# Kernel optimization log

Hardware: AMD Instinct MI355X
Metric: run time of the kernel (lower is better)

The kernel has to match this reference:

```python
import jax, jax.numpy as jnp
import numpy as np

DIM = 1024
HEADS = 16
HEAD_DIM = DIM // HEADS          # 64
ROT_DIM = max(16, HEAD_DIM // 2) # 32 (already even)
B, S = 1, 2048


def _linear_params(key, scale=0.02):
    w = jax.random.normal(key, (DIM, DIM), dtype=jnp.float32) * scale
    b = jnp.zeros((DIM,), dtype=jnp.float32)
    return w, b


def setup_inputs() -> dict:
    key = jax.random.key(0)
    ks = jax.random.split(key, 16)
    real = jax.random.normal(ks[0], (B, S, DIM), dtype=jnp.float32)
    imag = jax.random.normal(ks[1], (B, S, DIM), dtype=jnp.float32)
    Wq_r, bq_r = _linear_params(ks[2])
    Wk_r, bk_r = _linear_params(ks[3])
    Wv_r, bv_r = _linear_params(ks[4])
    Wq_i, bq_i = _linear_params(ks[5])
    Wk_i, bk_i = _linear_params(ks[6])
    Wv_i, bv_i = _linear_params(ks[7])
    Wo_r, bo_r = _linear_params(ks[8])
    Wo_i, bo_i = _linear_params(ks[9])
    phase_shifts = jax.random.normal(ks[10], (HEADS, HEAD_DIM), dtype=jnp.float32) * 0.02
    # entanglement init: 0.8*I + 0.1 on super/sub diagonal + 0.1 corners
    ent = np.eye(HEADS, dtype=np.float32) * 0.8
    ent += np.diag(np.ones(HEADS - 1, dtype=np.float32) * 0.1, k=1)
    ent += np.diag(np.ones(HEADS - 1, dtype=np.float32) * 0.1, k=-1)
    ent[0, -1] = 0.1
    ent[-1, 0] = 0.1
    entanglement_matrix = jnp.asarray(ent)
    exponent = np.arange(0, ROT_DIM, 2, dtype=np.float64) / ROT_DIM
    rotary_freqs = jnp.asarray((10000.0 ** (-exponent)).astype(np.float32))
    return {
        'real': real, 'imag': imag,
        'Wq_r': Wq_r, 'bq_r': bq_r, 'Wk_r': Wk_r, 'bk_r': bk_r,
        'Wv_r': Wv_r, 'bv_r': bv_r, 'Wq_i': Wq_i, 'bq_i': bq_i,
        'Wk_i': Wk_i, 'bk_i': bk_i, 'Wv_i': Wv_i, 'bv_i': bv_i,
        'Wo_r': Wo_r, 'bo_r': bo_r, 'Wo_i': Wo_i, 'bo_i': bo_i,
        'phase_shifts': phase_shifts,
        'entanglement_matrix': entanglement_matrix,
        'rotary_freqs': rotary_freqs,
        'interference_strength': jnp.float32(0.0),
        'attention_temperature': jnp.float32(0.0),
        'circle_epsilon': jnp.float32(-2.0),
    }


def _proj(x, W, b):
    # nn.Linear: x @ W^T + b, then split heads -> [B,H,S,Dh]
    y = x @ W.T + b
    return y.reshape(B, S, HEADS, HEAD_DIM).transpose(0, 2, 1, 3)


def _rope(x, cos, sin):
    # x: [B,H,S,Dh]; interleaved pairs rotated over first ROT_DIM dims
    xr, xp = x[..., :ROT_DIM], x[..., ROT_DIM:]
    x1, x2 = xr[..., 0::2], xr[..., 1::2]          # [B,H,S,ROT_DIM//2]
    o1 = x1 * cos - x2 * sin
    o2 = x1 * sin + x2 * cos
    out = jnp.stack([o1, o2], axis=-1).reshape(x.shape[:-1] + (ROT_DIM,))
    return jnp.concatenate([out, xp], axis=-1)


def reference(real, imag, Wq_r, bq_r, Wk_r, bk_r, Wv_r, bv_r,
              Wq_i, bq_i, Wk_i, bk_i, Wv_i, bv_i,
              Wo_r, bo_r, Wo_i, bo_i,
              phase_shifts, entanglement_matrix, rotary_freqs,
              interference_strength, attention_temperature, circle_epsilon):
    q_r = _proj(real, Wq_r, bq_r)
    k_r = _proj(real, Wk_r, bk_r)
    v_r = _proj(real, Wv_r, bv_r)
    q_i = _proj(imag, Wq_i, bq_i)
    k_i = _proj(imag, Wk_i, bk_i)
    v_i = _proj(imag, Wv_i, bv_i)

    # rotary embeddings
    pos = jnp.arange(S, dtype=jnp.float32)
    angles = jnp.outer(pos, rotary_freqs)              # [S, ROT_DIM//2]
    cos = jnp.cos(angles)[None, None]                  # [1,1,S,ROT_DIM//2]
    sin = jnp.sin(angles)[None, None]
    q_r = _rope(q_r, cos, sin); k_r = _rope(k_r, cos, sin)
    q_i = _rope(q_i, cos, sin); k_i = _rope(k_i, cos, sin)

    # entanglement mixing across heads
    q_r = jnp.einsum('bhsd,hx->bxsd', q_r, entanglement_matrix)
    q_i = jnp.einsum('bhsd,hx->bxsd', q_i, entanglement_matrix)
    k_r = jnp.einsum('bhsd,hx->bxsd', k_r, entanglement_matrix)
    k_i = jnp.einsum('bhsd,hx->bxsd', k_i, entanglement_matrix)

    # per-head learned phase shift
    pc = jnp.cos(phase_shifts)[None, :, None, :]       # [1,H,1,Dh]
    ps = jnp.sin(phase_shifts)[None, :, None, :]
    q_r, q_i = q_r * pc - q_i * ps, q_r * ps + q_i * pc
    k_r, k_i = k_r * pc - k_i * ps, k_r * ps + k_i * pc

    # complex attention scores (Karatsuba, as in HAKMEMComplexOperations)
    scale = 1.0 / np.sqrt(HEAD_DIM)
    k1 = jnp.einsum('bhsd,bhtd->bhst', q_r, k_r)
    k2 = jnp.einsum('bhsd,bhtd->bhst', q_i, k_i)
    k3 = jnp.einsum('bhsd,bhtd->bhst', q_r + q_i, k_r + k_i)
    attn_r = (k1 - k2) * scale
    attn_i = (k3 - k1 - k2) * scale

    eps = jax.nn.sigmoid(circle_epsilon) * 0.03
    ar = attn_r + eps * attn_i
    ai = attn_i - eps * attn_r
    attn_mag = jnp.sqrt(ar * ar + ai * ai + 1e-6)

    causal = jnp.triu(jnp.ones((S, S), dtype=bool), k=1)[None, None]
    attn_mag = jnp.where(causal, -jnp.inf, attn_mag)

    temp = jnp.clip(jnp.exp(attention_temperature), 0.1, None)
    strength = jax.nn.sigmoid(interference_strength)
    attn = jax.nn.softmax(attn_mag * strength / temp, axis=-1)
    attn = jnp.nan_to_num(attn)

    # complex_matmul(attn, 0, v_r, v_i) -> (attn@v_r, attn@v_i)
    out_r = jnp.einsum('bhst,bhtd->bhsd', attn, v_r)
    out_i = jnp.einsum('bhst,bhtd->bhsd', attn, v_i)
    out_r = out_r.transpose(0, 2, 1, 3).reshape(B, S, DIM)
    out_i = out_i.transpose(0, 2, 1, 3).reshape(B, S, DIM)
    out_r = out_r @ Wo_r.T + bo_r
    out_i = out_i @ Wo_i.T + bo_i
    return out_r, out_i
```

## Files before the change

### kernel.cpp

```cpp
#include <hip/hip_runtime.h>
#include <cstddef>
#include <cstdint>
#include <math.h>

#define S_LEN 2048
#define DIM 1024
#define NH 16
#define HD 64

typedef __attribute__((ext_vector_type(8))) short bf16x8;
typedef __attribute__((ext_vector_type(8))) unsigned short u16x8;
typedef __attribute__((ext_vector_type(4))) float f32x4;

__device__ inline unsigned short f2bf(float x) {
  union { float f; unsigned u; } v; v.f = x;
  unsigned r = v.u + 0x7FFFu + ((v.u >> 16) & 1u);
  return (unsigned short)(r >> 16);
}
__device__ inline float bf2f(unsigned short x) {
  union { unsigned u; float f; } v; v.u = ((unsigned)x) << 16; return v.f;
}
__device__ inline unsigned pack_bf16_trunc(float hi, float lo) {
  union { float f; unsigned u; } a, b;
  a.f = hi; b.f = lo;
  return __builtin_amdgcn_perm(a.u, b.u, 0x07060302u);
}

#define GLOAD_LDS16(g, l)                                              \
  __builtin_amdgcn_global_load_lds(                                    \
      (const __attribute__((address_space(1))) void*)(g),              \
      (__attribute__((address_space(3))) void*)(l), 16, 0, 0)

struct ConvBatch {
  const float* src[6];
  unsigned short* dst[6];
  int n[6];
};

__global__ __launch_bounds__(256) void conv_kernel(
    ConvBatch cb, const float* __restrict__ E,
    const float* __restrict__ freqs, const float* __restrict__ phase,
    const float* __restrict__ bq_r, const float* __restrict__ bk_r,
    const float* __restrict__ bq_i, const float* __restrict__ bk_i,
    float* __restrict__ biasf, float2* __restrict__ ropeTab,
    float2* __restrict__ phaseTab2)
{
  const int t = threadIdx.x;
  const int y = blockIdx.y;

  if (y == 6) {
    __shared__ float Es[NH * NH];
    Es[t] = E[t];
    __syncthreads();
    const int idx = blockIdx.x * 256 + t;
    if (idx < 32768) {
      const int s = idx >> 4, j = idx & 15;
      float sn, cs;
      sincosf((float)s * freqs[j], &sn, &cs);
      ropeTab[idx] = make_float2(cs, sn);
    } else if (idx < 32768 + 1024) {
      const int k = idx - 32768;
      float sn, cs;
      sincosf(2.f * phase[k], &sn, &cs);
      phaseTab2[k] = make_float2(cs, sn);
    } else if (idx < 32768 + 1024 + 4096) {
      const int i = idx - 33792;
      const int tz = i >> 10, nn = i & 1023;
      const int x = nn >> 6, d = nn & 63;
      const float* b = (tz == 0) ? bq_r : (tz == 1) ? bk_r : (tz == 2) ? bq_i : bk_i;
      float acc = 0.f;
#pragma unroll
      for (int h = 0; h < NH; h++) acc += Es[h * NH + x] * b[h * 64 + d];
      biasf[i] = acc;
    }
    return;
  }

  const int flat = (blockIdx.x * 256 + t) * 8;
  if (flat >= cb.n[y]) return;
  const float* s = cb.src[y];
  float4 a = *(const float4*)(s + flat);
  float4 b = *(const float4*)(s + flat + 4);
  u16x8 o;
  o[0] = f2bf(a.x); o[1] = f2bf(a.y); o[2] = f2bf(a.z); o[3] = f2bf(a.w);
  o[4] = f2bf(b.x); o[5] = f2bf(b.y); o[6] = f2bf(b.z); o[7] = f2bf(b.w);
  *(u16x8*)(cb.dst[y] + flat) = o;
}

__global__ __launch_bounds__(256) void fold_kernel(
    const float* __restrict__ Wq_r, const float* __restrict__ Wk_r,
    const float* __restrict__ Wq_i, const float* __restrict__ Wk_i,
    unsigned short* __restrict__ Wb, const float* __restrict__ E)
{
  __shared__ float Es[NH * NH];
  const int t = threadIdx.x;
  Es[t] = E[t];
  __syncthreads();

  const int d  = blockIdx.x;
  const int wi = blockIdx.y;
  const float* src = (wi == 0) ? Wq_r : (wi == 1) ? Wk_r : (wi == 2) ? Wq_i : Wk_i;
  const int slot   = (wi == 0) ? 0 : (wi == 1) ? 1 : (wi == 2) ? 3 : 4;
  unsigned short* dst = Wb + (size_t)slot * DIM * DIM;

  const int k0 = t * 4;
  float4 in[NH];
#pragma unroll
  for (int h = 0; h < NH; h++)
    in[h] = *(const float4*)(src + ((size_t)(h * 64 + d) << 10) + k0);

#pragma unroll
  for (int x = 0; x < NH; x++) {
    float ax = 0.f, ay = 0.f, az = 0.f, aw = 0.f;
#pragma unroll
    for (int h = 0; h < NH; h++) {
      const float e = Es[h * NH + x];
      ax += e * in[h].x; ay += e * in[h].y;
      az += e * in[h].z; aw += e * in[h].w;
    }
    ushort4 o;
    o.x = f2bf(ax); o.y = f2bf(ay); o.z = f2bf(az); o.w = f2bf(aw);
    *(ushort4*)(dst + ((size_t)(x * 64 + d) << 10) + k0) = o;
  }
}

struct BGemm {
  const unsigned short* A[6];
  const unsigned short* W[6];
  const float* bias[6];
  void* C[6];
  int mode[6];
  const float2* ropeTab;
};

__global__ __launch_bounds__(256) void gemm_mfma_kernel(BGemm gb)
{
  constexpr int K = DIM;
  const int z = blockIdx.z;
  const unsigned short* __restrict__ A = gb.A[z];
  const unsigned short* __restrict__ W = gb.W[z];
  const float* __restrict__ bias = gb.bias[z];
  const int mode = gb.mode[z];

  __shared__ __align__(16) unsigned short As[128 * 32];
  __shared__ __align__(16) unsigned short Ws[128 * 32];

  const int t    = threadIdx.x;
  const int lane = t & 63;
  const int w    = t >> 6;
  const int wm   = w >> 1, wn = w & 1;
  const int quad = lane >> 4, lcol = lane & 15;
  const int m0   = blockIdx.y * 128;
  const int n0   = blockIdx.x * 128;

  const int srow = t >> 2;
  const int sk8  = (t & 3) * 8;

  f32x4 acc[4][4];
#pragma unroll
  for (int i = 0; i < 4; i++)
#pragma unroll
    for (int j = 0; j < 4; j++)
#pragma unroll
      for (int r = 0; r < 4; r++) acc[i][j][r] = 0.f;

  for (int k0 = 0; k0 < K; k0 += 32) {
    __syncthreads();
#pragma unroll
    for (int p = 0; p < 2; p++) {
      const unsigned short* ga = A + (size_t)(m0 + p * 64 + srow) * K + k0 + sk8;
      GLOAD_LDS16(ga, As + (size_t)(p * 256 + w * 64) * 8);
      const unsigned short* gw = W + (size_t)(n0 + p * 64 + srow) * K + k0 + sk8;
      GLOAD_LDS16(gw, Ws + (size_t)(p * 256 + w * 64) * 8);
    }
    __syncthreads();

    bf16x8 af[4], bfr[4];
#pragma unroll
    for (int mi = 0; mi < 4; mi++)
      af[mi] = *(const bf16x8*)&As[(wm * 64 + mi * 16 + lcol) * 32 + quad * 8];
#pragma unroll
    for (int ni = 0; ni < 4; ni++)
      bfr[ni] = *(const bf16x8*)&Ws[(wn * 64 + ni * 16 + lcol) * 32 + quad * 8];
#pragma unroll
    for (int mi = 0; mi < 4; mi++)
#pragma unroll
      for (int ni = 0; ni < 4; ni++)
        acc[mi][ni] = __builtin_amdgcn_mfma_f32_16x16x32_bf16(af[mi], bfr[ni], acc[mi][ni], 0, 0, 0);
  }

#pragma unroll
  for (int mi = 0; mi < 4; mi++) {
#pragma unroll
    for (int ni = 0; ni < 4; ni++) {
#pragma unroll
      for (int r = 0; r < 4; r++) {
        const int grow = m0 + wm * 64 + mi * 16 + quad * 4 + r;
        const int gcol = n0 + wn * 64 + ni * 16 + lcol;
        float v = acc[mi][ni][r] + bias[gcol];
        if (mode == 3) {
          const float vp = __shfl_xor(v, 1);
          const int d = gcol & 63;
          if (d < 32) {
            const float2 cs = gb.ropeTab[grow * 16 + (d >> 1)];
            v = (d & 1) ? (v * cs.x + vp * cs.y)
                        : (v * cs.x - vp * cs.y);
          }
        }
        if (mode == 0) {
          ((float*)gb.C[z])[(size_t)grow * DIM + gcol] = v;
        } else if (mode == 2) {
          const int hh = gcol >> 6, d = gcol & 63;
          ((unsigned short*)gb.C[z])[((size_t)hh * HD + d) * S_LEN + grow] = f2bf(v);
        } else {
          const int hh = gcol >> 6, d = gcol & 63;
          ((unsigned short*)gb.C[z])[((size_t)hh * S_LEN + grow) * HD + d] = f2bf(v);
        }
      }
    }
  }
}

#define LDK 72

__global__ __launch_bounds__(256) void flash_mfma_kernel(
    const unsigned short* __restrict__ Qr, const unsigned short* __restrict__ Qi,
    const unsigned short* __restrict__ Kr, const unsigned short* __restrict__ Ki,
    const unsigned short* __restrict__ VtR, const unsigned short* __restrict__ VtI,
    unsigned short* __restrict__ OpR, unsigned short* __restrict__ OpI,
    float* __restrict__ Lp, const float2* __restrict__ phaseTab2,
    const float* __restrict__ p_is, const float* __restrict__ p_at,
    const float* __restrict__ p_ce)
{
  __shared__ __align__(16) unsigned short Krs[64 * LDK];
  __shared__ __align__(16) unsigned short Kis[64 * LDK];
  __shared__ __align__(16) unsigned short VTr[64 * LDK];
  __shared__ __align__(16) unsigned short VTi[64 * LDK];
  unsigned short* Ps = Krs;

  const int t    = threadIdx.x;
  const int lane = t & 63;
  const int w    = t >> 6;
  const int quad = lane >> 4;
  const int lcol = lane & 15;

  const int bx    = blockIdx.x;
  const int p     = bx >> 1;
  const int half  = bx & 1;
  const int itile = 31 - (p >> 4);
  const int h     = p & 15;
  const int i0    = itile * 64;
  const int n     = itile + 1;
  const int jmid  = (n + 1) >> 1;
  const int jbeg  = half ? jmid : 0;
  const int jend  = half ? n : jmid;

  const float strength = 1.f / (1.f + expf(-p_is[0]));
  const float temp     = fmaxf(expf(p_at[0]), 0.1f);
  const float cfac     = strength / temp;
  const float eps      = 0.03f / (1.f + expf(-p_ce[0]));
  const float c2       = 0.015625f * (1.f + eps * eps);
  const float cl       = cfac * 1.4426950408889634f;
  const float c2e      = c2 * cl * cl;
  const float epse     = 1e-6f * cl * cl;

  const int srow = t >> 3;
  const int sd0  = (t & 7) * 8;

  const int qg = i0 + w * 16 + lcol;

  bf16x8 qrf[2], qif[2];
  {
    const size_t base_q = ((size_t)h * S_LEN + qg) * HD;
#pragma unroll
    for (int ks = 0; ks < 2; ks++) {
      bf16x8 r8 = *(const bf16x8*)(Qr + base_q + ks * 32 + quad * 8);
      bf16x8 i8 = *(const bf16x8*)(Qi + base_q + ks * 32 + quad * 8);
      bf16x8 orr, oii;
#pragma unroll
      for (int j = 0; j < 8; j++) {
        const float2 ph = phaseTab2[h * HD + ks * 32 + quad * 8 + j];
        const float qr = bf2f((unsigned short)r8[j]);
        const float qi = bf2f((unsigned short)i8[j]);
        orr[j] = (short)f2bf(qr * ph.x - qi * ph.y);
        oii[j] = (short)f2bf(qr * ph.y + qi * ph.x);
      }
      qrf[ks] = orr;
      qif[ks] = oii;
    }
  }

  float lsum = 0.f;
  f32x4 aOr[4], aOi[4];
#pragma unroll
  for (int cc = 0; cc < 4; cc++)
#pragma unroll
    for (int r = 0; r < 4; r++) { aOr[cc][r] = 0.f; aOi[cc][r] = 0.f; }

  bf16x8 pk[2], pki[2], pv[2], pvi[2];

  const unsigned short* pKr = Kr  + ((size_t)h * S_LEN + jbeg * 64 + srow) * HD + sd0;
  const unsigned short* pKi = Ki  + ((size_t)h * S_LEN + jbeg * 64 + srow) * HD + sd0;
  const unsigned short* pVr = VtR + ((size_t)h * HD + srow) * S_LEN + jbeg * 64 + sd0;
  const unsigned short* pVi = VtI + ((size_t)h * HD + srow) * S_LEN + jbeg * 64 + sd0;

  if (jbeg < jend) {
#pragma unroll
    for (int it = 0; it < 2; it++) {
      pk [it] = *(const bf16x8*)(pKr + (size_t)it * 32 * HD);
      pki[it] = *(const bf16x8*)(pKi + (size_t)it * 32 * HD);
      pv [it] = *(const bf16x8*)(pVr + (size_t)it * 32 * S_LEN);
      pvi[it] = *(const bf16x8*)(pVi + (size_t)it * 32 * S_LEN);
    }
  }

  for (int jt = jbeg; jt < jend; jt++) {
    __syncthreads();
#pragma unroll
    for (int it = 0; it < 2; it++) {
      const int row = srow + it * 32;
      *(bf16x8*)&Krs[row * LDK + sd0] = pk [it];
      *(bf16x8*)&Kis[row * LDK + sd0] = pki[it];
      *(bf16x8*)&VTr[row * LDK + sd0] = pv [it];
      *(bf16x8*)&VTi[row * LDK + sd0] = pvi[it];
    }
    __syncthreads();

    if (jt + 1 < jend) {
      pKr += 64 * HD; pKi += 64 * HD; pVr += 64; pVi += 64;
#pragma unroll
      for (int it = 0; it < 2; it++) {
        pk [it] = *(const bf16x8*)(pKr + (size_t)it * 32 * HD);
        pki[it] = *(const bf16x8*)(pKi + (size_t)it * 32 * HD);
        pv [it] = *(const bf16x8*)(pVr + (size_t)it * 32 * S_LEN);
        pvi[it] = *(const bf16x8*)(pVi + (size_t)it * 32 * S_LEN);
      }
    }

    f32x4 k1[4], k2[4], kx[4];
#pragma unroll
    for (int cc = 0; cc < 4; cc++)
#pragma unroll
      for (int r = 0; r < 4; r++) { k1[cc][r] = 0.f; k2[cc][r] = 0.f; kx[cc][r] = 0.f; }
#pragma unroll
    for (int ks = 0; ks < 2; ks++) {
#pragma unroll
      for (int cc = 0; cc < 4; cc++) {
        const int off = (cc * 16 + lcol) * LDK + ks * 32 + quad * 8;
        bf16x8 krf = *(const bf16x8*)&Krs[off];
        bf16x8 kif = *(const bf16x8*)&Kis[off];
        k1[cc] = __builtin_amdgcn_mfma_f32_16x16x32_bf16(krf, qrf[ks], k1[cc], 0, 0, 0);
        k2[cc] = __builtin_amdgcn_mfma_f32_16x16x32_bf16(kif, qif[ks], k2[cc], 0, 0, 0);
        kx[cc] = __builtin_amdgcn_mfma_f32_16x16x32_bf16(kif, qrf[ks], kx[cc], 0, 0, 0);
        kx[cc] = __builtin_amdgcn_mfma_f32_16x16x32_bf16(krf, qif[ks], kx[cc], 0, 0, 0);
      }
    }

    __syncthreads();

    const int prow = (w * 16 + lcol) * LDK;
    if (jt != itile) {
#pragma unroll
      for (int cc = 0; cc < 4; cc++) {
        float pv4[4];
#pragma unroll
        for (int r = 0; r < 4; r++) {
          const float a = k1[cc][r] - k2[cc][r];
          const float b = kx[cc][r];
          const float u = fmaf(b, b, a * a);
          const float pp = __builtin_amdgcn_exp2f(sqrtf(fmaf(u, c2e, epse)));
          pv4[r] = pp;
          lsum += pp;
        }
        uint2 packed;
        packed.x = pack_bf16_trunc(pv4[1], pv4[0]);
        packed.y = pack_bf16_trunc(pv4[3], pv4[2]);
        *(uint2*)&Ps[prow + cc * 16 + quad * 4] = packed;
      }
    } else {
      const int j0 = jt * 64;
#pragma unroll
      for (int cc = 0; cc < 4; cc++) {
        float pv4[4];
#pragma unroll
        for (int r = 0; r < 4; r++) {
          const float a = k1[cc][r] - k2[cc][r];
          const float b = kx[cc][r];
          const float u = fmaf(b, b, a * a);
          float pp = __builtin_amdgcn_exp2f(sqrtf(fmaf(u, c2e, epse)));
          const int gj = j0 + cc * 16 + quad * 4 + r;
          if (gj > qg) pp = 0.f;
          pv4[r] = pp;
          lsum += pp;
        }
        uint2 packed;
        packed.x = pack_bf16_trunc(pv4[1], pv4[0]);
        packed.y = pack_bf16_trunc(pv4[3], pv4[2]);
        *(uint2*)&Ps[prow + cc * 16 + quad * 4] = packed;
      }
    }

#pragma unroll
    for (int ks = 0; ks < 2; ks++) {
      bf16x8 pf = *(const bf16x8*)&Ps[(w * 16 + lcol) * LDK + ks * 32 + quad * 8];
#pragma unroll
      for (int cc = 0; cc < 4; cc++) {
        const int off = (cc * 16 + lcol) * LDK + ks * 32 + quad * 8;
        bf16x8 vrf = *(const bf16x8*)&VTr[off];
        bf16x8 vif = *(const bf16x8*)&VTi[off];
        aOr[cc] = __builtin_amdgcn_mfma_f32_16x16x32_bf16(vrf, pf, aOr[cc], 0, 0, 0);
        aOi[cc] = __builtin_amdgcn_mfma_f32_16x16x32_bf16(vif, pf, aOi[cc], 0, 0, 0);
      }
    }
  }

  lsum += __shfl_xor(lsum, 16);
  lsum += __shfl_xor(lsum, 32);
  if (lane < 16)
    Lp[((size_t)half * NH + h) * S_LEN + qg] = lsum;

  const size_t SLsz = (size_t)S_LEN * DIM;
  const size_t rowbase = half * SLsz + (size_t)qg * DIM + h * HD;
#pragma unroll
  for (int cc = 0; cc < 4; cc++) {
    const int d0 = cc * 16 + quad * 4;
    uint2 pr, pi;
    pr.x = pack_bf16_trunc(aOr[cc][1], aOr[cc][0]);
    pr.y = pack_bf16_trunc(aOr[cc][3], aOr[cc][2]);
    pi.x = pack_bf16_trunc(aOi[cc][1], aOi[cc][0]);
    pi.y = pack_bf16_trunc(aOi[cc][3], aOi[cc][2]);
    *(uint2*)(OpR + rowbase + d0) = pr;
    *(uint2*)(OpI + rowbase + d0) = pi;
  }
}

__global__ __launch_bounds__(256) void combine_kernel(
    const unsigned short* __restrict__ OpR, const unsigned short* __restrict__ OpI,
    const float* __restrict__ Lp,
    unsigned short* __restrict__ Or, unsigned short* __restrict__ Oi)
{
  const size_t SLsz = (size_t)S_LEN * DIM;
  const int idx = blockIdx.x * 256 + threadIdx.x;
  const size_t e0 = (size_t)idx * 8;
  const int s = (int)(e0 >> 10);
  const int col = (int)(e0 & 1023);
  const int h = col >> 6;

  const float L = Lp[(size_t)h * S_LEN + s] + Lp[((size_t)NH + h) * S_LEN + s];
  const float inv = 1.f / L;

  bf16x8 r0 = *(const bf16x8*)(OpR + e0);
  bf16x8 r1 = *(const bf16x8*)(OpR + SLsz + e0);
  bf16x8 i0 = *(const bf16x8*)(OpI + e0);
  bf16x8 i1 = *(const bf16x8*)(OpI + SLsz + e0);

  u16x8 orv, oiv;
#pragma unroll
  for (int j = 0; j < 8; j++) {
    orv[j] = f2bf((bf2f((unsigned short)r0[j]) + bf2f((unsigned short)r1[j])) * inv);
    oiv[j] = f2bf((bf2f((unsigned short)i0[j]) + bf2f((unsigned short)i1[j])) * inv);
  }
  *(u16x8*)(Or + e0) = orv;
  *(u16x8*)(Oi + e0) = oiv;
}

extern "C" void kernel_launch(void* const* d_in, const int* in_sizes, int n_in,
                              void* d_out, int out_size, void* d_ws, size_t ws_size,
                              hipStream_t stream)
{
  const float* real = (const float*)d_in[0];
  const float* imag = (const float*)d_in[1];
  const float* Wq_r = (const float*)d_in[2];
  const float* bq_r = (const float*)d_in[3];
  const float* Wk_r = (const float*)d_in[4];
  const float* bk_r = (const float*)d_in[5];
  const float* Wv_r = (const float*)d_in[6];
  const float* bv_r = (const float*)d_in[7];
  const float* Wq_i = (const float*)d_in[8];
  const float* bq_i = (const float*)d_in[9];
  const float* Wk_i = (const float*)d_in[10];
  const float* bk_i = (const float*)d_in[11];
  const float* Wv_i = (const float*)d_in[12];
  const float* bv_i = (const float*)d_in[13];
  const float* Wo_r = (const float*)d_in[14];
  const float* bo_r = (const float*)d_in[15];
  const float* Wo_i = (const float*)d_in[16];
  const float* bo_i = (const float*)d_in[17];
  const float* phase = (const float*)d_in[18];
  const float* ent   = (const float*)d_in[19];
  const float* freqs = (const float*)d_in[20];
  const float* p_is  = (const float*)d_in[21];
  const float* p_at  = (const float*)d_in[22];
  const float* p_ce  = (const float*)d_in[23];

  unsigned short* ws = (unsigned short*)d_ws;
  const size_t SL = (size_t)S_LEN * DIM;
  const size_t WL = (size_t)DIM * DIM;

  unsigned short* realb = ws;
  unsigned short* imagb = realb + SL;
  unsigned short* Wb    = imagb + SL;
  unsigned short* q_r   = Wb + 8 * WL;
  unsigned short* k_r   = q_r + SL;
  unsigned short* v_r   = k_r + SL;
  unsigned short* q_i   = v_r + SL;
  unsigned short* k_i   = q_i + SL;
  unsigned short* v_i   = k_i + SL;
  unsigned short* OpR   = v_i + SL;
  unsigned short* OpI   = OpR + 2 * SL;

  float* fbase    = (float*)(OpI + 2 * SL);
  float* biasf    = fbase;
  float* ropeTab  = biasf + 4096;
  float* phaseTb2 = ropeTab + 65536;
  float* Lp       = phaseTb2 + 2048;

  unsigned short* O_r = q_r;
  unsigned short* O_i = q_i;

  float* out_r = (float*)d_out;
  float* out_i = out_r + SL;

  ConvBatch cb;
  cb.src[0] = real;  cb.dst[0] = realb;        cb.n[0] = (int)SL;
  cb.src[1] = imag;  cb.dst[1] = imagb;        cb.n[1] = (int)SL;
  cb.src[2] = Wv_r;  cb.dst[2] = Wb + 2 * WL;  cb.n[2] = (int)WL;
  cb.src[3] = Wv_i;  cb.dst[3] = Wb + 5 * WL;  cb.n[3] = (int)WL;
  cb.src[4] = Wo_r;  cb.dst[4] = Wb + 6 * WL;  cb.n[4] = (int)WL;
  cb.src[5] = Wo_i;  cb.dst[5] = Wb + 7 * WL;  cb.n[5] = (int)WL;
  conv_kernel<<<dim3(1024, 7), dim3(256), 0, stream>>>(
      cb, ent, freqs, phase, bq_r, bk_r, bq_i, bk_i,
      biasf, (float2*)ropeTab, (float2*)phaseTb2);

  fold_kernel<<<dim3(64, 4), dim3(256), 0, stream>>>(
      Wq_r, Wk_r, Wq_i, Wk_i, Wb, ent);

  BGemm g1;
  g1.A[0] = realb; g1.A[1] = realb; g1.A[2] = realb;
  g1.A[3] = imagb; g1.A[4] = imagb; g1.A[5] = imagb;
  for (int i = 0; i < 6; i++) g1.W[i] = Wb + (size_t)i * WL;
  g1.bias[0] = biasf;        g1.bias[1] = biasf + 1024; g1.bias[2] = bv_r;
  g1.bias[3] = biasf + 2048; g1.bias[4] = biasf + 3072; g1.bias[5] = bv_i;
  g1.C[0] = q_r; g1.C[1] = k_r; g1.C[2] = v_r;
  g1.C[3] = q_i; g1.C[4] = k_i; g1.C[5] = v_i;
  g1.mode[0] = 3; g1.mode[1] = 3; g1.mode[2] = 2;
  g1.mode[3] = 3; g1.mode[4] = 3; g1.mode[5] = 2;
  g1.ropeTab = (const float2*)ropeTab;
  gemm_mfma_kernel<<<dim3(8, 16, 6), dim3(256), 0, stream>>>(g1);

  flash_mfma_kernel<<<dim3(1024), dim3(256), 0, stream>>>(
      q_r, q_i, k_r, k_i, v_r, v_i, OpR, OpI, Lp,
      (const float2*)phaseTb2, p_is, p_at, p_ce);

  combine_kernel<<<dim3(1024), dim3(256), 0, stream>>>(OpR, OpI, Lp, O_r, O_i);

  BGemm g2 = {};
  g2.A[0] = O_r; g2.A[1] = O_i;
  g2.W[0] = Wb + 6 * WL; g2.W[1] = Wb + 7 * WL;
  g2.bias[0] = bo_r; g2.bias[1] = bo_i;
  g2.C[0] = out_r; g2.C[1] = out_i;
  g2.mode[0] = 0; g2.mode[1] = 0;
  g2.ropeTab = (const float2*)ropeTab;
  gemm_mfma_kernel<<<dim3(8, 16, 2), dim3(256), 0, stream>>>(g2);
}
```

Before: 275.0 us.

## Fuse weight fold into conv kernel and split-K combine into flash kernel

The separate fold kernel becomes extra grid rows of the conversion kernel, and the combine kernel is removed. The second flash block to finish each tile pair now merges the two partial outputs, coordinated through a per-tile atomic counter. This drops two kernel launches and a full pass over the partial outputs, at the cost of a memset, thread fences, atomics and a serial tail in the last-finishing block. O_r/O_i move to dedicated workspace buffers instead of reusing q_r/q_i.

```diff
diff --git a/kernel.cpp b/kernel.cpp
--- a/kernel.cpp
+++ b/kernel.cpp
@@ -42,6 +42,9 @@
     const float* __restrict__ freqs, const float* __restrict__ phase,
     const float* __restrict__ bq_r, const float* __restrict__ bk_r,
     const float* __restrict__ bq_i, const float* __restrict__ bk_i,
+    const float* __restrict__ Wq_r, const float* __restrict__ Wk_r,
+    const float* __restrict__ Wq_i, const float* __restrict__ Wk_i,
+    unsigned short* __restrict__ Wb,
     float* __restrict__ biasf, float2* __restrict__ ropeTab,
     float2* __restrict__ phaseTab2)
 {
@@ -76,6 +79,39 @@
     return;
   }
 
+  if (y >= 7) {
+    if (blockIdx.x >= 64) return;
+    __shared__ float Es2[NH * NH];
+    Es2[t] = E[t];
+    __syncthreads();
+    const int d  = blockIdx.x;
+    const int wi = y - 7;
+    const float* src = (wi == 0) ? Wq_r : (wi == 1) ? Wk_r : (wi == 2) ? Wq_i : Wk_i;
+    const int slot   = (wi == 0) ? 0 : (wi == 1) ? 1 : (wi == 2) ? 3 : 4;
+    unsigned short* dst = Wb + (size_t)slot * DIM * DIM;
+
+    const int k0 = t * 4;
+    float4 in[NH];
+#pragma unroll
+    for (int h = 0; h < NH; h++)
+      in[h] = *(const float4*)(src + ((size_t)(h * 64 + d) << 10) + k0);
+
+#pragma unroll
+    for (int x = 0; x < NH; x++) {
+      float ax = 0.f, ay = 0.f, az = 0.f, aw = 0.f;
+#pragma unroll
+      for (int h = 0; h < NH; h++) {
+        const float e = Es2[h * NH + x];
+        ax += e * in[h].x; ay += e * in[h].y;
+        az += e * in[h].z; aw += e * in[h].w;
+      }
+      ushort4 o;
+      o.x = f2bf(ax); o.y = f2bf(ay); o.z = f2bf(az); o.w = f2bf(aw);
+      *(ushort4*)(dst + ((size_t)(x * 64 + d) << 10) + k0) = o;
+    }
+    return;
+  }
+
   const int flat = (blockIdx.x * 256 + t) * 8;
   if (flat >= cb.n[y]) return;
   const float* s = cb.src[y];
@@ -85,43 +121,6 @@
   o[0] = f2bf(a.x); o[1] = f2bf(a.y); o[2] = f2bf(a.z); o[3] = f2bf(a.w);
   o[4] = f2bf(b.x); o[5] = f2bf(b.y); o[6] = f2bf(b.z); o[7] = f2bf(b.w);
   *(u16x8*)(cb.dst[y] + flat) = o;
-}
-
-__global__ __launch_bounds__(256) void fold_kernel(
-    const float* __restrict__ Wq_r, const float* __restrict__ Wk_r,
-    const float* __restrict__ Wq_i, const float* __restrict__ Wk_i,
-    unsigned short* __restrict__ Wb, const float* __restrict__ E)
-{
-  __shared__ float Es[NH * NH];
-  const int t = threadIdx.x;
-  Es[t] = E[t];
-  __syncthreads();
-
-  const int d  = blockIdx.x;
-  const int wi = blockIdx.y;
-  const float* src = (wi == 0) ? Wq_r : (wi == 1) ? Wk_r : (wi == 2) ? Wq_i : Wk_i;
-  const int slot   = (wi == 0) ? 0 : (wi == 1) ? 1 : (wi == 2) ? 3 : 4;
-  unsigned short* dst = Wb + (size_t)slot * DIM * DIM;
-
-  const int k0 = t * 4;
-  float4 in[NH];
-#pragma unroll
-  for (int h = 0; h < NH; h++)
-    in[h] = *(const float4*)(src + ((size_t)(h * 64 + d) << 10) + k0);
-
-#pragma unroll
-  for (int x = 0; x < NH; x++) {
-    float ax = 0.f, ay = 0.f, az = 0.f, aw = 0.f;
-#pragma unroll
-    for (int h = 0; h < NH; h++) {
-      const float e = Es[h * NH + x];
-      ax += e * in[h].x; ay += e * in[h].y;
-      az += e * in[h].z; aw += e * in[h].w;
-    }
-    ushort4 o;
-    o.x = f2bf(ax); o.y = f2bf(ay); o.z = f2bf(az); o.w = f2bf(aw);
-    *(ushort4*)(dst + ((size_t)(x * 64 + d) << 10) + k0) = o;
-  }
 }
 
 struct BGemm {
@@ -228,7 +227,9 @@
     const unsigned short* __restrict__ Kr, const unsigned short* __restrict__ Ki,
     const unsigned short* __restrict__ VtR, const unsigned short* __restrict__ VtI,
     unsigned short* __restrict__ OpR, unsigned short* __restrict__ OpI,
-    float* __restrict__ Lp, const float2* __restrict__ phaseTab2,
+    float* __restrict__ Lp, int* __restrict__ flags,
+    unsigned short* __restrict__ Or, unsigned short* __restrict__ Oi,
+    const float2* __restrict__ phaseTab2,
     const float* __restrict__ p_is, const float* __restrict__ p_at,
     const float* __restrict__ p_ce)
 {
@@ -432,36 +433,34 @@
     *(uint2*)(OpR + rowbase + d0) = pr;
     *(uint2*)(OpI + rowbase + d0) = pi;
   }
-}
-
-__global__ __launch_bounds__(256) void combine_kernel(
-    const unsigned short* __restrict__ OpR, const unsigned short* __restrict__ OpI,
-    const float* __restrict__ Lp,
-    unsigned short* __restrict__ Or, unsigned short* __restrict__ Oi)
-{
-  const size_t SLsz = (size_t)S_LEN * DIM;
-  const int idx = blockIdx.x * 256 + threadIdx.x;
-  const size_t e0 = (size_t)idx * 8;
-  const int s = (int)(e0 >> 10);
-  const int col = (int)(e0 & 1023);
-  const int h = col >> 6;
-
-  const float L = Lp[(size_t)h * S_LEN + s] + Lp[((size_t)NH + h) * S_LEN + s];
-  const float inv = 1.f / L;
-
-  bf16x8 r0 = *(const bf16x8*)(OpR + e0);
-  bf16x8 r1 = *(const bf16x8*)(OpR + SLsz + e0);
-  bf16x8 i0 = *(const bf16x8*)(OpI + e0);
-  bf16x8 i1 = *(const bf16x8*)(OpI + SLsz + e0);
-
-  u16x8 orv, oiv;
-#pragma unroll
-  for (int j = 0; j < 8; j++) {
-    orv[j] = f2bf((bf2f((unsigned short)r0[j]) + bf2f((unsigned short)r1[j])) * inv);
-    oiv[j] = f2bf((bf2f((unsigned short)i0[j]) + bf2f((unsigned short)i1[j])) * inv);
-  }
-  *(u16x8*)(Or + e0) = orv;
-  *(u16x8*)(Oi + e0) = oiv;
+
+  __threadfence();
+  __shared__ int sOld;
+  if (t == 0) sOld = atomicAdd(&flags[p], 1);
+  __syncthreads();
+  if (sOld == 1) {
+    __threadfence();
+    for (int idx = t; idx < 64 * 8; idx += 256) {
+      const int row = i0 + (idx >> 3);
+      const int d0  = (idx & 7) * 8;
+      const float L = Lp[(size_t)h * S_LEN + row] +
+                      Lp[((size_t)NH + h) * S_LEN + row];
+      const float inv = 1.f / L;
+      const size_t off = (size_t)row * DIM + h * HD + d0;
+      bf16x8 r0 = *(const bf16x8*)(OpR + off);
+      bf16x8 r1 = *(const bf16x8*)(OpR + SLsz + off);
+      bf16x8 i0v = *(const bf16x8*)(OpI + off);
+      bf16x8 i1v = *(const bf16x8*)(OpI + SLsz + off);
+      u16x8 orv, oiv;
+#pragma unroll
+      for (int j = 0; j < 8; j++) {
+        orv[j] = f2bf((bf2f((unsigned short)r0[j]) + bf2f((unsigned short)r1[j])) * inv);
+        oiv[j] = f2bf((bf2f((unsigned short)i0v[j]) + bf2f((unsigned short)i1v[j])) * inv);
+      }
+      *(u16x8*)(Or + off) = orv;
+      *(u16x8*)(Oi + off) = oiv;
+    }
+  }
 }
 
 extern "C" void kernel_launch(void* const* d_in, const int* in_sizes, int n_in,
@@ -508,18 +507,20 @@
   unsigned short* v_i   = k_i + SL;
   unsigned short* OpR   = v_i + SL;
   unsigned short* OpI   = OpR + 2 * SL;
-
-  float* fbase    = (float*)(OpI + 2 * SL);
+  unsigned short* O_r   = OpI + 2 * SL;
+  unsigned short* O_i   = O_r + SL;
+
+  float* fbase    = (float*)(O_i + SL);
   float* biasf    = fbase;
   float* ropeTab  = biasf + 4096;
   float* phaseTb2 = ropeTab + 65536;
   float* Lp       = phaseTb2 + 2048;
-
-  unsigned short* O_r = q_r;
-  unsigned short* O_i = q_i;
+  int*   flags    = (int*)(Lp + 2 * NH * S_LEN);
 
   float* out_r = (float*)d_out;
   float* out_i = out_r + SL;
+
+  hipMemsetAsync(flags, 0, 512 * sizeof(int), stream);
 
   ConvBatch cb;
   cb.src[0] = real;  cb.dst[0] = realb;        cb.n[0] = (int)SL;
@@ -528,12 +529,10 @@
   cb.src[3] = Wv_i;  cb.dst[3] = Wb + 5 * WL;  cb.n[3] = (int)WL;
   cb.src[4] = Wo_r;  cb.dst[4] = Wb + 6 * WL;  cb.n[4] = (int)WL;
   cb.src[5] = Wo_i;  cb.dst[5] = Wb + 7 * WL;  cb.n[5] = (int)WL;
-  conv_kernel<<<dim3(1024, 7), dim3(256), 0, stream>>>(
+  conv_kernel<<<dim3(1024, 11), dim3(256), 0, stream>>>(
       cb, ent, freqs, phase, bq_r, bk_r, bq_i, bk_i,
+      Wq_r, Wk_r, Wq_i, Wk_i, Wb,
       biasf, (float2*)ropeTab, (float2*)phaseTb2);
-
-  fold_kernel<<<dim3(64, 4), dim3(256), 0, stream>>>(
-      Wq_r, Wk_r, Wq_i, Wk_i, Wb, ent);
 
   BGemm g1;
   g1.A[0] = realb; g1.A[1] = realb; g1.A[2] = realb;
@@ -549,10 +548,8 @@
   gemm_mfma_kernel<<<dim3(8, 16, 6), dim3(256), 0, stream>>>(g1);
 
   flash_mfma_kernel<<<dim3(1024), dim3(256), 0, stream>>>(
-      q_r, q_i, k_r, k_i, v_r, v_i, OpR, OpI, Lp,
+      q_r, q_i, k_r, k_i, v_r, v_i, OpR, OpI, Lp, flags, O_r, O_i,
       (const float2*)phaseTb2, p_is, p_at, p_ce);
-
-  combine_kernel<<<dim3(1024), dim3(256), 0, stream>>>(OpR, OpI, Lp, O_r, O_i);
 
   BGemm g2 = {};
   g2.A[0] = O_r; g2.A[1] = O_i;
```

Result: slower. 501.1 us (+82.2%).
